# Kernel optimization log

Measured on AMD Instinct MI355X. Metric: run time of the kernel, lower is better.

## Reference

```python
import jax, jax.numpy as jnp
import numpy as np

B, S, E, H = 1, 2048, 512, 8
D = E // H
N = B * S
WIN_HALF = 32  # attention_window 64 -> +/-32
ALPHA = 0.1
LN_EPS = 1e-12
NEG_INF = -1e9


def _build_window_edges():
    # windowed graph: dst i attends to src j with |i-j| <= WIN_HALF, within each batch block
    i = np.arange(S)
    offs = np.arange(-WIN_HALF, WIN_HALF + 1)
    src = i[:, None] + offs[None, :]
    dst = np.broadcast_to(i[:, None], src.shape)
    valid = (src >= 0) & (src < S)
    src, dst = src[valid], dst[valid]
    srcs, dsts = [], []
    for b in range(B):
        srcs.append(src + b * S)
        dsts.append(dst + b * S)
    return (np.concatenate(srcs).astype(np.int32),
            np.concatenate(dsts).astype(np.int32))


def setup_inputs() -> dict:
    key = jax.random.key(0)
    ks = jax.random.split(key, 12)
    sc = 1.0 / np.sqrt(E)
    src_np, dst_np = _build_window_edges()
    return {
        "hidden_states": jax.random.normal(ks[0], (B, S, E), dtype=jnp.float32),
        "attention_mask": jnp.zeros((B, S), dtype=jnp.float32),
        "edge_src": jnp.asarray(src_np),
        "edge_dst": jnp.asarray(dst_np),
        "Wq": jax.random.normal(ks[1], (E, E), dtype=jnp.float32) * sc,
        "bq": jnp.zeros((E,), dtype=jnp.float32),
        "Wk": jax.random.normal(ks[2], (E, E), dtype=jnp.float32) * sc,
        "bk": jnp.zeros((E,), dtype=jnp.float32),
        "Wv": jax.random.normal(ks[3], (E, E), dtype=jnp.float32) * sc,
        "bv": jnp.zeros((E,), dtype=jnp.float32),
        "Wo": jax.random.normal(ks[4], (E, E), dtype=jnp.float32) * sc,
        "bo": jnp.zeros((E,), dtype=jnp.float32),
        "ln_g": jnp.ones((E,), dtype=jnp.float32),
        "ln_b": jnp.zeros((E,), dtype=jnp.float32),
    }


def reference(hidden_states, attention_mask, edge_src, edge_dst,
              Wq, bq, Wk, bk, Wv, bv, Wo, bo, ln_g, ln_b):
    x = hidden_states  # (B,S,E); node ordering n = b*S + s (matches torch reshape)
    q = ((x @ Wq + bq) / jnp.sqrt(jnp.asarray(D, x.dtype))).reshape(N, H, D)
    k = (x @ Wk + bk).reshape(N, H, D)
    v = (x @ Wv + bv).reshape(N, H, D)

    mask = (attention_mask >= 0).reshape(N)  # bool per node

    # u_dot_v('k','q','score'): per-edge, per-head dot product
    score = jnp.einsum('ehd,ehd->eh', k[edge_src], q[edge_dst])  # (Eg,H)
    score = jnp.where(mask[edge_src][:, None], score, NEG_INF)

    # edge_softmax over incoming edges of each destination node
    smax = jax.ops.segment_max(score, edge_dst, num_segments=N)
    p = jnp.exp(score - smax[edge_dst])
    denom = jax.ops.segment_sum(p, edge_dst, num_segments=N)
    p = p / denom[edge_dst]  # (Eg,H)

    # 5 diffusion steps: h <- A h, blended with residual v (dropout off in eval)
    h = v
    for _ in range(5):
        m = h[edge_src] * p[:, :, None]                      # u_mul_e
        h = jax.ops.segment_sum(m, edge_dst, num_segments=N)  # sum('m','h')
        h = (1.0 - ALPHA) * h + ALPHA * v

    attn = h.reshape(B, S, E)

    # DiffuserSelfOutput: dense -> residual add -> LayerNorm
    y = attn @ Wo + bo + hidden_states
    mu = y.mean(-1, keepdims=True)
    var = ((y - mu) ** 2).mean(-1, keepdims=True)
    out = (y - mu) * jax.lax.rsqrt(var + LN_EPS) * ln_g + ln_b
    return out
```

## Files before the change

### kernel.cpp

```cpp
#include <hip/hip_runtime.h>
#include <math.h>

#define S_LEN 2048
#define E_DIM 512
#define NE (S_LEN * E_DIM)
#define H_NUM 8
#define WH 32
#define NOFF 65
#define PROW (H_NUM * NOFF)
#define PN (S_LEN * PROW)

typedef float f32x4 __attribute__((ext_vector_type(4)));
typedef short short8 __attribute__((ext_vector_type(8)));

__device__ __forceinline__ unsigned short f2bf(float f) {
    union { float f; unsigned u; } cv; cv.f = f;
    unsigned u = cv.u;
    u += 0x7fffu + ((u >> 16) & 1u);
    return (unsigned short)(u >> 16);
}
__device__ __forceinline__ unsigned pk2(float x, float y) {
    return (unsigned)f2bf(x) | ((unsigned)f2bf(y) << 16);
}

__device__ __forceinline__ void mfma_gemm_f32(
    const float* __restrict__ A, const float* __restrict__ W,
    const float* __restrict__ bias, float* __restrict__ C,
    float scale, int m0, int n0)
{
    __shared__ unsigned short As[64 * 40];
    __shared__ unsigned short Bs[64 * 40];
    const int tid = threadIdx.x;
    const int lane = tid & 63, wave = tid >> 6;
    const int quad = lane >> 4, l16 = lane & 15;
    const int wr = (wave >> 1) * 32, wc = (wave & 1) * 32;
    const int ar = tid >> 2, ac = (tid & 3) * 8;
    const int bn = tid & 63, bk0 = (tid >> 6) * 8;

    f32x4 acc00 = {0.f,0.f,0.f,0.f}, acc01 = acc00, acc10 = acc00, acc11 = acc00;

    for (int kk = 0; kk < E_DIM; kk += 32) {
        float4 a0 = *(const float4*)(A + (size_t)(m0 + ar) * E_DIM + kk + ac);
        float4 a1 = *(const float4*)(A + (size_t)(m0 + ar) * E_DIM + kk + ac + 4);
        float b[8];
#pragma unroll
        for (int j = 0; j < 8; ++j)
            b[j] = W[(size_t)(kk + bk0 + j) * E_DIM + n0 + bn];
        __syncthreads();
        uint4 ap; ap.x = pk2(a0.x, a0.y); ap.y = pk2(a0.z, a0.w);
        ap.z = pk2(a1.x, a1.y); ap.w = pk2(a1.z, a1.w);
        *(uint4*)(As + ar * 40 + ac) = ap;
        uint4 bp; bp.x = pk2(b[0], b[1]); bp.y = pk2(b[2], b[3]);
        bp.z = pk2(b[4], b[5]); bp.w = pk2(b[6], b[7]);
        *(uint4*)(Bs + bn * 40 + bk0) = bp;
        __syncthreads();
        short8 fa0 = *(const short8*)(As + (wr + l16) * 40 + quad * 8);
        short8 fa1 = *(const short8*)(As + (wr + 16 + l16) * 40 + quad * 8);
        short8 fb0 = *(const short8*)(Bs + (wc + l16) * 40 + quad * 8);
        short8 fb1 = *(const short8*)(Bs + (wc + 16 + l16) * 40 + quad * 8);
        acc00 = __builtin_amdgcn_mfma_f32_16x16x32_bf16(fa0, fb0, acc00, 0, 0, 0);
        acc01 = __builtin_amdgcn_mfma_f32_16x16x32_bf16(fa0, fb1, acc01, 0, 0, 0);
        acc10 = __builtin_amdgcn_mfma_f32_16x16x32_bf16(fa1, fb0, acc10, 0, 0, 0);
        acc11 = __builtin_amdgcn_mfma_f32_16x16x32_bf16(fa1, fb1, acc11, 0, 0, 0);
    }

#pragma unroll
    for (int mi = 0; mi < 2; ++mi) {
#pragma unroll
        for (int ni = 0; ni < 2; ++ni) {
            f32x4 a = (mi == 0) ? ((ni == 0) ? acc00 : acc01)
                                : ((ni == 0) ? acc10 : acc11);
            int n = n0 + wc + ni * 16 + l16;
            float bval = bias[n];
#pragma unroll
            for (int r = 0; r < 4; ++r) {
                int m = m0 + wr + mi * 16 + quad * 4 + r;
                C[(size_t)m * E_DIM + n] = (a[r] + bval) * scale;
            }
        }
    }
}

__global__ __launch_bounds__(256)
void qkv_gemm(const float* __restrict__ x,
              const float* __restrict__ Wq, const float* __restrict__ bq,
              const float* __restrict__ Wk, const float* __restrict__ bk,
              const float* __restrict__ Wv, const float* __restrict__ bv,
              float* __restrict__ q, float* __restrict__ k, float* __restrict__ v)
{
    const float* W; const float* b; float* o; float sc;
    if (blockIdx.z == 0)      { W = Wq; b = bq; o = q; sc = 0.125f; }
    else if (blockIdx.z == 1) { W = Wk; b = bk; o = k; sc = 1.0f; }
    else                      { W = Wv; b = bv; o = v; sc = 1.0f; }
    mfma_gemm_f32(x, W, b, o, sc, blockIdx.y * 64, blockIdx.x * 64);
}

#define SDN 32
__global__ __launch_bounds__(256)
void scores_d1(const float* __restrict__ q, const float* __restrict__ k,
               const float* __restrict__ v, const float* __restrict__ amask,
               float* __restrict__ P, float* __restrict__ hA)
{
    const int i0 = blockIdx.x * SDN;
    const int h  = blockIdx.y;
    const int tid = threadIdx.x;
    __shared__ float ks[96 * 68];
    __shared__ float am[96];
    __shared__ float sc[SDN * 66];
    __shared__ float smx[SDN], sidn[SDN];
    __shared__ float ps[SDN * NOFF];

    for (int e = tid; e < 96 * 16; e += 256) {
        int lr = e >> 4, c4 = e & 15;
        int j = i0 - WH + lr;
        int jc = min(max(j, 0), S_LEN - 1);
        *(float4*)(ks + lr * 68 + c4 * 4) =
            *(const float4*)(k + (size_t)jc * E_DIM + h * 64 + c4 * 4);
    }
    if (tid < 96) {
        int j = i0 - WH + tid;
        am[tid] = (j >= 0 && j < S_LEN) ? amask[j] : -1.0f;
    }

    const int dst = tid >> 3;
    const int og  = tid & 7;
    float4 qreg[16];
    {
        const float4* qrow = (const float4*)(q + (size_t)(i0 + dst) * E_DIM + h * 64);
#pragma unroll
        for (int t = 0; t < 16; ++t) qreg[t] = qrow[t];
    }
    __syncthreads();

    for (int off = og; off < NOFF; off += 8) {
        int j = i0 + dst + off - WH;
        float s;
        if (j < 0 || j >= S_LEN) {
            s = -INFINITY;
        } else {
            int lr = dst + off;
            const float4* kr = (const float4*)(ks + lr * 68);
            float acc = 0.f;
#pragma unroll
            for (int t = 0; t < 16; ++t) {
                float4 a = qreg[t], bb = kr[t];
                acc += a.x * bb.x + a.y * bb.y + a.z * bb.z + a.w * bb.w;
            }
            s = (am[lr] >= 0.f) ? acc : -1e9f;
        }
        sc[dst * 66 + off] = s;
    }
    __syncthreads();

    for (int e = tid; e < 96 * 16; e += 256) {
        int lr = e >> 4, c4 = e & 15;
        int j = i0 - WH + lr;
        int jc = min(max(j, 0), S_LEN - 1);
        *(float4*)(ks + lr * 68 + c4 * 4) =
            *(const float4*)(v + (size_t)jc * E_DIM + h * 64 + c4 * 4);
    }
    if (tid < SDN) {
        float mx = -INFINITY;
        for (int o = 0; o < NOFF; ++o) mx = fmaxf(mx, sc[tid * 66 + o]);
        float dn = 0.f;
        for (int o = 0; o < NOFF; ++o) dn += expf(sc[tid * 66 + o] - mx);
        smx[tid] = mx; sidn[tid] = 1.f / dn;
    }
    __syncthreads();

    for (int e = tid; e < SDN * NOFF; e += 256) {
        int d = e / NOFF, off = e - d * NOFF;
        float pv = expf(sc[d * 66 + off] - smx[d]) * sidn[d];
        P[(size_t)(i0 + d) * PROW + h * NOFF + off] = pv;
        ps[e] = pv;
    }
    __syncthreads();

    {
        const int ci = tid & 15;
        const int ob = (tid >> 4) * 2;
        float4 a0 = {0,0,0,0}, a1 = a0;
        for (int lr = ob; lr < ob + 66; ++lr) {
            float4 hval = *(const float4*)(ks + lr * 68 + ci * 4);
            int o0 = lr - ob;
            if (o0 <= 64) {
                float p = ps[ob * NOFF + o0];
                a0.x += p * hval.x; a0.y += p * hval.y; a0.z += p * hval.z; a0.w += p * hval.w;
            }
            int o1 = o0 - 1;
            if ((unsigned)o1 <= 64u) {
                float p = ps[(ob + 1) * NOFF + o1];
                a1.x += p * hval.x; a1.y += p * hval.y; a1.z += p * hval.z; a1.w += p * hval.w;
            }
        }
#pragma unroll
        for (int r = 0; r < 2; ++r) {
            float4 a = r ? a1 : a0;
            float4 vv = *(const float4*)(ks + (WH + ob + r) * 68 + ci * 4);
            float4 o;
            o.x = 0.9f * a.x + 0.1f * vv.x;
            o.y = 0.9f * a.y + 0.1f * vv.y;
            o.z = 0.9f * a.z + 0.1f * vv.z;
            o.w = 0.9f * a.w + 0.1f * vv.w;
            *(float4*)(hA + (size_t)(i0 + ob + r) * E_DIM + h * 64 + ci * 4) = o;
        }
    }
}

__global__ __launch_bounds__(512)
void diffuse3m(const float* __restrict__ hin, const float* __restrict__ v,
               const float* __restrict__ P, float* __restrict__ hout)
{
    __shared__ unsigned short inT[64 * 264];
    __shared__ unsigned short m1T[64 * 200];
    __shared__ unsigned short ps[192 * 66];
    unsigned short* m2T = inT;
    const int i0 = blockIdx.x * 64;
    const int h  = blockIdx.y;
    const int c0 = h * 64;
    const int tid  = threadIdx.x;
    const int lane = tid & 63, wave = tid >> 6;
    const int quad = lane >> 4, l16 = lane & 15;

    for (int e = tid; e < 128 * 16; e += 512) {
        int rp = (e >> 4) * 2, c4 = (e & 15) * 4;
        int ja = min(max(i0 - 96 + rp,     0), S_LEN - 1);
        int jb = min(max(i0 - 96 + rp + 1, 0), S_LEN - 1);
        float4 ha = *(const float4*)(hin + (size_t)ja * E_DIM + c0 + c4);
        float4 hb = *(const float4*)(hin + (size_t)jb * E_DIM + c0 + c4);
        *(unsigned*)(inT + (c4 + 0) * 264 + rp) = pk2(ha.x, hb.x);
        *(unsigned*)(inT + (c4 + 1) * 264 + rp) = pk2(ha.y, hb.y);
        *(unsigned*)(inT + (c4 + 2) * 264 + rp) = pk2(ha.z, hb.z);
        *(unsigned*)(inT + (c4 + 3) * 264 + rp) = pk2(ha.w, hb.w);
    }
    for (int e = tid; e < 192 * 33; e += 512) {
        int mr = e / 33, t = e - mr * 33;
        int jc = min(max(i0 - 64 + mr, 0), S_LEN - 1);
        const float* pr = P + (size_t)jc * PROW + h * NOFF;
        if (t < 32)
            *(unsigned*)(ps + mr * 66 + t * 2) = pk2(pr[t * 2], pr[t * 2 + 1]);
        else
            ps[mr * 66 + 64] = f2bf(pr[64]);
    }
    __syncthreads();

#pragma unroll
    for (int uu = 0; uu < 3; ++uu) {
        int u = wave + uu * 8;
        int mtb = (u >> 1) * 16;
        int ntb = (u & 1) * 32;
        f32x4 a0 = {0.f,0.f,0.f,0.f}, a1 = a0;
        int ks0 = mtb >> 5;
        const int m = mtb + l16;
#pragma unroll
        for (int t = 0; t < 3; ++t) {
            int k0q = (ks0 + t) * 32 + quad * 8;
            short8 fa;
#pragma unroll
            for (int j = 0; j < 8; ++j) {
                int idx = k0q + j - m;
                int idc = min(max(idx, 0), 64);
                unsigned short pv = ps[m * 66 + idc];
                fa[j] = ((unsigned)idx <= 64u) ? (short)pv : (short)0;
            }
            short8 fb0 = *(const short8*)(inT + (ntb + l16) * 264 + k0q);
            short8 fb1 = *(const short8*)(inT + (ntb + 16 + l16) * 264 + k0q);
            a0 = __builtin_amdgcn_mfma_f32_16x16x32_bf16(fa, fb0, a0, 0, 0, 0);
            a1 = __builtin_amdgcn_mfma_f32_16x16x32_bf16(fa, fb1, a1, 0, 0, 0);
        }
#pragma unroll
        for (int nt = 0; nt < 2; ++nt) {
            f32x4 a = nt ? a1 : a0;
            int n = ntb + nt * 16 + l16;
            float o[4];
#pragma unroll
            for (int r = 0; r < 4; ++r) {
                int gm = min(max(i0 - 64 + mtb + quad * 4 + r, 0), S_LEN - 1);
                o[r] = 0.9f * a[r] + 0.1f * v[(size_t)gm * E_DIM + c0 + n];
            }
            *(unsigned*)(m1T + n * 200 + mtb + quad * 4)     = pk2(o[0], o[1]);
            *(unsigned*)(m1T + n * 200 + mtb + quad * 4 + 2) = pk2(o[2], o[3]);
        }
    }
    __syncthreads();

#pragma unroll
    for (int uu = 0; uu < 2; ++uu) {
        int u = wave + uu * 8;
        int mtb = (u >> 1) * 16;
        int ntb = (u & 1) * 32;
        f32x4 a0 = {0.f,0.f,0.f,0.f}, a1 = a0;
        int ks0 = mtb >> 5;
        const int m = mtb + l16;
#pragma unroll
        for (int t = 0; t < 3; ++t) {
            int k0q = (ks0 + t) * 32 + quad * 8;
            short8 fa;
#pragma unroll
            for (int j = 0; j < 8; ++j) {
                int idx = k0q + j - m;
                int idc = min(max(idx, 0), 64);
                unsigned short pv = ps[(m + 32) * 66 + idc];
                fa[j] = ((unsigned)idx <= 64u) ? (short)pv : (short)0;
            }
            short8 fb0 = *(const short8*)(m1T + (ntb + l16) * 200 + k0q);
            short8 fb1 = *(const short8*)(m1T + (ntb + 16 + l16) * 200 + k0q);
            a0 = __builtin_amdgcn_mfma_f32_16x16x32_bf16(fa, fb0, a0, 0, 0, 0);
            a1 = __builtin_amdgcn_mfma_f32_16x16x32_bf16(fa, fb1, a1, 0, 0, 0);
        }
        __syncthreads();
#pragma unroll
        for (int nt = 0; nt < 2; ++nt) {
            f32x4 a = nt ? a1 : a0;
            int n = ntb + nt * 16 + l16;
            float o[4];
#pragma unroll
            for (int r = 0; r < 4; ++r) {
                int gm = min(max(i0 - 32 + mtb + quad * 4 + r, 0), S_LEN - 1);
                o[r] = 0.9f * a[r] + 0.1f * v[(size_t)gm * E_DIM + c0 + n];
            }
            *(unsigned*)(m2T + n * 136 + mtb + quad * 4)     = pk2(o[0], o[1]);
            *(unsigned*)(m2T + n * 136 + mtb + quad * 4 + 2) = pk2(o[2], o[3]);
        }
    }
    __syncthreads();

    {
        int u = wave;
        int mtb = (u >> 1) * 16;
        int ntb = (u & 1) * 32;
        f32x4 a0 = {0.f,0.f,0.f,0.f}, a1 = a0;
        int ks0 = mtb >> 5;
        const int m = mtb + l16;
#pragma unroll
        for (int t = 0; t < 3; ++t) {
            int k0q = (ks0 + t) * 32 + quad * 8;
            short8 fa;
#pragma unroll
            for (int j = 0; j < 8; ++j) {
                int idx = k0q + j - m;
                int idc = min(max(idx, 0), 64);
                unsigned short pv = ps[(m + 64) * 66 + idc];
                fa[j] = ((unsigned)idx <= 64u) ? (short)pv : (short)0;
            }
            short8 fb0 = *(const short8*)(m2T + (ntb + l16) * 136 + k0q);
            short8 fb1 = *(const short8*)(m2T + (ntb + 16 + l16) * 136 + k0q);
            a0 = __builtin_amdgcn_mfma_f32_16x16x32_bf16(fa, fb0, a0, 0, 0, 0);
            a1 = __builtin_amdgcn_mfma_f32_16x16x32_bf16(fa, fb1, a1, 0, 0, 0);
        }
#pragma unroll
        for (int nt = 0; nt < 2; ++nt) {
            f32x4 a = nt ? a1 : a0;
            int n = ntb + nt * 16 + l16;
#pragma unroll
            for (int r = 0; r < 4; ++r) {
                int gm = i0 + mtb + quad * 4 + r;
                size_t base = (size_t)gm * E_DIM + c0 + n;
                hout[base] = 0.9f * a[r] + 0.1f * v[base];
            }
        }
    }
}

__global__ __launch_bounds__(512)
void oln4(const float* __restrict__ h4, const float* __restrict__ v,
          const float* __restrict__ P, const float* __restrict__ Wo,
          const float* __restrict__ bo, const float* __restrict__ x,
          const float* __restrict__ g, const float* __restrict__ lb,
          float* __restrict__ out)
{
    __shared__ unsigned short As16[16 * 520];
    __shared__ unsigned short Bs2[2][512 * 40];
    __shared__ float rsum[8][16], rsq[8][16];
    unsigned short* h4T  = &Bs2[0][0];
    unsigned short* ps16 = &Bs2[0][0] + 26624;

    const int tid = threadIdx.x;
    const int lane = tid & 63, wave = tid >> 6;
    const int quad = lane >> 4, l16 = lane & 15;
    const int m0 = blockIdx.x * 16;
    const int n = tid;

    for (int e = tid; e < 16 * 260; e += 512) {
        int mr = e / 260, t = e - mr * 260;
        const float* pr = P + (size_t)(m0 + mr) * PROW;
        *(unsigned*)(ps16 + mr * 528 + t * 2) = pk2(pr[t * 2], pr[t * 2 + 1]);
    }

    for (int hc = 0; hc < 2; ++hc) {
        for (int e = tid; e < 64 * 64; e += 512) {
            int r = e & 63, c4 = (e >> 6) * 4;
            int row = min(max(m0 - 32 + r, 0), S_LEN - 1);
            float4 hv = *(const float4*)(h4 + (size_t)row * E_DIM + hc * 256 + c4);
            h4T[(c4 + 0) * 104 + r] = f2bf(hv.x);
            h4T[(c4 + 1) * 104 + r] = f2bf(hv.y);
            h4T[(c4 + 2) * 104 + r] = f2bf(hv.z);
            h4T[(c4 + 3) * 104 + r] = f2bf(hv.w);
        }
        for (int e = tid; e < 32 * 64; e += 512) {
            int r = 64 + (e & 31), c4 = (e >> 5) * 4;
            int row = min(max(m0 - 32 + r, 0), S_LEN - 1);
            float4 hv = *(const float4*)(h4 + (size_t)row * E_DIM + hc * 256 + c4);
            h4T[(c4 + 0) * 104 + r] = f2bf(hv.x);
            h4T[(c4 + 1) * 104 + r] = f2bf(hv.y);
            h4T[(c4 + 2) * 104 + r] = f2bf(hv.z);
            h4T[(c4 + 3) * 104 + r] = f2bf(hv.w);
        }
        __syncthreads();

        {
            const int hd = hc * 4 + (wave >> 1);
            short8 fa[3];
#pragma unroll
            for (int t = 0; t < 3; ++t) {
                int k0q = t * 32 + quad * 8;
#pragma unroll
                for (int j = 0; j < 8; ++j) {
                    int idx = k0q + j - l16;
                    int idc = min(max(idx, 0), 64);
                    unsigned short pv = ps16[l16 * 528 + hd * NOFF + idc];
                    fa[t][j] = ((unsigned)idx <= 64u) ? (short)pv : (short)0;
                }
            }
#pragma unroll
            for (int nt = 0; nt < 2; ++nt) {
                int lc = wave * 32 + nt * 16;
                f32x4 ba = {0.f, 0.f, 0.f, 0.f};
#pragma unroll
                for (int t = 0; t < 3; ++t) {
                    short8 fb = *(const short8*)(h4T + (lc + l16) * 104 + t * 32 + quad * 8);
                    ba = __builtin_amdgcn_mfma_f32_16x16x32_bf16(fa[t], fb, ba, 0, 0, 0);
                }
                int gcol = hc * 256 + lc + l16;
#pragma unroll
                for (int r = 0; r < 4; ++r) {
                    int m = quad * 4 + r;
                    float vv = v[(size_t)(m0 + m) * E_DIM + gcol];
                    As16[m * 520 + gcol] = f2bf(0.9f * ba[r] + 0.1f * vv);
                }
            }
        }
        __syncthreads();
    }

    {
        float w0[32];
#pragma unroll
        for (int j = 0; j < 32; ++j)
            w0[j] = Wo[(size_t)j * E_DIM + n];
#pragma unroll
        for (int t = 0; t < 4; ++t) {
            uint4 bp;
            bp.x = pk2(w0[t*8+0], w0[t*8+1]); bp.y = pk2(w0[t*8+2], w0[t*8+3]);
            bp.z = pk2(w0[t*8+4], w0[t*8+5]); bp.w = pk2(w0[t*8+6], w0[t*8+7]);
            *(uint4*)(&Bs2[0][0] + n * 40 + t * 8) = bp;
        }
    }

    f32x4 acc[4];
#pragma unroll
    for (int t = 0; t < 4; ++t) acc[t] = (f32x4){0.f,0.f,0.f,0.f};

#pragma unroll 2
    for (int it = 0; it < 16; ++it) {
        float wn[32];
        if (it < 15) {
#pragma unroll
            for (int j = 0; j < 32; ++j)
                wn[j] = Wo[(size_t)((it + 1) * 32 + j) * E_DIM + n];
        }
        __syncthreads();

        short8 fa = *(const short8*)(As16 + l16 * 520 + it * 32 + quad * 8);
#pragma unroll
        for (int nt = 0; nt < 4; ++nt) {
            short8 fb = *(const short8*)(&Bs2[it & 1][0] +
                                         (wave * 64 + nt * 16 + l16) * 40 + quad * 8);
            acc[nt] = __builtin_amdgcn_mfma_f32_16x16x32_bf16(fa, fb, acc[nt], 0, 0, 0);
        }

        if (it < 15) {
#pragma unroll
            for (int t = 0; t < 4; ++t) {
                uint4 bp;
                bp.x = pk2(wn[t*8+0], wn[t*8+1]); bp.y = pk2(wn[t*8+2], wn[t*8+3]);
                bp.z = pk2(wn[t*8+4], wn[t*8+5]); bp.w = pk2(wn[t*8+6], wn[t*8+7]);
                *(uint4*)(&Bs2[(it + 1) & 1][0] + n * 40 + t * 8) = bp;
            }
        }
    }

    float s[4] = {0.f,0.f,0.f,0.f}, s2[4] = {0.f,0.f,0.f,0.f};
#pragma unroll
    for (int nt = 0; nt < 4; ++nt) {
        int nc = wave * 64 + nt * 16 + l16;
        float bv = bo[nc];
#pragma unroll
        for (int r = 0; r < 4; ++r) {
            int m = m0 + quad * 4 + r;
            float vl = acc[nt][r] + bv + x[(size_t)m * E_DIM + nc];
            acc[nt][r] = vl;
            s[r] += vl; s2[r] += vl * vl;
        }
    }
#pragma unroll
    for (int o = 1; o < 16; o <<= 1) {
#pragma unroll
        for (int r = 0; r < 4; ++r) {
            s[r]  += __shfl_xor(s[r], o, 64);
            s2[r] += __shfl_xor(s2[r], o, 64);
        }
    }
    if (l16 == 0) {
#pragma unroll
        for (int r = 0; r < 4; ++r) {
            rsum[wave][quad * 4 + r] = s[r];
            rsq[wave][quad * 4 + r]  = s2[r];
        }
    }
    __syncthreads();
    float mu[4], rs[4];
#pragma unroll
    for (int r = 0; r < 4; ++r) {
        int rl = quad * 4 + r;
        float tot = 0.f, tot2 = 0.f;
#pragma unroll
        for (int w = 0; w < 8; ++w) { tot += rsum[w][rl]; tot2 += rsq[w][rl]; }
        float m_ = tot * (1.f / 512.f);
        float var = tot2 * (1.f / 512.f) - m_ * m_;
        mu[r] = m_; rs[r] = rsqrtf(var + 1e-12f);
    }
#pragma unroll
    for (int nt = 0; nt < 4; ++nt) {
        int nc = wave * 64 + nt * 16 + l16;
        float gv = g[nc], bbv = lb[nc];
#pragma unroll
        for (int r = 0; r < 4; ++r) {
            int m = m0 + quad * 4 + r;
            out[(size_t)m * E_DIM + nc] = (acc[nt][r] - mu[r]) * rs[r] * gv + bbv;
        }
    }
}

extern "C" void kernel_launch(void* const* d_in, const int* in_sizes, int n_in,
                              void* d_out, int out_size, void* d_ws, size_t ws_size,
                              hipStream_t stream)
{
    const float* x     = (const float*)d_in[0];
    const float* amask = (const float*)d_in[1];
    const float* Wq = (const float*)d_in[4];
    const float* bq = (const float*)d_in[5];
    const float* Wk = (const float*)d_in[6];
    const float* bk = (const float*)d_in[7];
    const float* Wv = (const float*)d_in[8];
    const float* bv = (const float*)d_in[9];
    const float* Wo = (const float*)d_in[10];
    const float* bo = (const float*)d_in[11];
    const float* lng = (const float*)d_in[12];
    const float* lnb = (const float*)d_in[13];
    float* out = (float*)d_out;

    float* ws = (float*)d_ws;
    float* q  = ws;
    float* k  = ws + (size_t)NE;
    float* v  = ws + (size_t)2 * NE;
    float* P  = ws + (size_t)3 * NE;
    float* hA = ws + (size_t)3 * NE + PN;
    float* hB = hA + (size_t)NE;

    qkv_gemm<<<dim3(8, 32, 3), 256, 0, stream>>>(x, Wq, bq, Wk, bk, Wv, bv, q, k, v);

    scores_d1<<<dim3(64, 8), 256, 0, stream>>>(q, k, v, amask, P, hA);

    diffuse3m<<<dim3(32, 8), 512, 0, stream>>>(hA, v, P, hB);

    oln4<<<128, 512, 0, stream>>>(hB, v, P, Wo, bo, x, lng, lnb, out);
}
```

Measured before the change: 170.7 us.

## Double-buffer QKV GEMM tiles, register-resident softmax, LDS-only barriers in output GEMM

The QKV projection GEMM now double-buffers its shared-memory tiles and prefetches global loads two iterations ahead, so each step needs one barrier that waits only on LDS operations. The scores kernel keeps scores in registers and computes the softmax max and sum with warp shuffles across the 8 lanes per destination, removing the shared score buffer, one barrier and the serial per-row loop. The output GEMM drops the barrier at the top of each iteration in favour of an LGKM-only barrier after the LDS writes, and fully unrolls the loop. The costs are higher register pressure from the prefetch buffers and unrolling, and the risk of ordering hazards if the custom barrier does not cover every outstanding memory operation.

```diff
diff --git a/kernel.cpp b/kernel.cpp
--- a/kernel.cpp
+++ b/kernel.cpp
@@ -23,13 +23,20 @@
     return (unsigned)f2bf(x) | ((unsigned)f2bf(y) << 16);
 }
 
+#define LGKM_BARRIER() do {                                   \
+    __builtin_amdgcn_sched_barrier(0);                        \
+    asm volatile("s_waitcnt lgkmcnt(0)" ::: "memory");        \
+    __builtin_amdgcn_s_barrier();                             \
+    __builtin_amdgcn_sched_barrier(0);                        \
+} while (0)
+
 __device__ __forceinline__ void mfma_gemm_f32(
     const float* __restrict__ A, const float* __restrict__ W,
     const float* __restrict__ bias, float* __restrict__ C,
     float scale, int m0, int n0)
 {
-    __shared__ unsigned short As[64 * 40];
-    __shared__ unsigned short Bs[64 * 40];
+    __shared__ unsigned short As[2][64 * 40];
+    __shared__ unsigned short Bs[2][64 * 40];
     const int tid = threadIdx.x;
     const int lane = tid & 63, wave = tid >> 6;
     const int quad = lane >> 4, l16 = lane & 15;
@@ -39,30 +46,58 @@
 
     f32x4 acc00 = {0.f,0.f,0.f,0.f}, acc01 = acc00, acc10 = acc00, acc11 = acc00;
 
-    for (int kk = 0; kk < E_DIM; kk += 32) {
-        float4 a0 = *(const float4*)(A + (size_t)(m0 + ar) * E_DIM + kk + ac);
-        float4 a1 = *(const float4*)(A + (size_t)(m0 + ar) * E_DIM + kk + ac + 4);
-        float b[8];
-#pragma unroll
-        for (int j = 0; j < 8; ++j)
-            b[j] = W[(size_t)(kk + bk0 + j) * E_DIM + n0 + bn];
-        __syncthreads();
-        uint4 ap; ap.x = pk2(a0.x, a0.y); ap.y = pk2(a0.z, a0.w);
-        ap.z = pk2(a1.x, a1.y); ap.w = pk2(a1.z, a1.w);
-        *(uint4*)(As + ar * 40 + ac) = ap;
-        uint4 bp; bp.x = pk2(b[0], b[1]); bp.y = pk2(b[2], b[3]);
-        bp.z = pk2(b[4], b[5]); bp.w = pk2(b[6], b[7]);
-        *(uint4*)(Bs + bn * 40 + bk0) = bp;
-        __syncthreads();
-        short8 fa0 = *(const short8*)(As + (wr + l16) * 40 + quad * 8);
-        short8 fa1 = *(const short8*)(As + (wr + 16 + l16) * 40 + quad * 8);
-        short8 fb0 = *(const short8*)(Bs + (wc + l16) * 40 + quad * 8);
-        short8 fb1 = *(const short8*)(Bs + (wc + 16 + l16) * 40 + quad * 8);
+    const float* Arow = A + (size_t)(m0 + ar) * E_DIM;
+
+    float4 a0r[2], a1r[2];
+    float  br[2][8];
+
+#define QLOAD(s_, i_) do {                                                    \
+        int kk_ = (i_) * 32;                                                  \
+        a0r[s_] = *(const float4*)(Arow + kk_ + ac);                          \
+        a1r[s_] = *(const float4*)(Arow + kk_ + ac + 4);                      \
+        _Pragma("unroll")                                                     \
+        for (int j_ = 0; j_ < 8; ++j_)                                        \
+            br[s_][j_] = W[(size_t)(kk_ + bk0 + j_) * E_DIM + n0 + bn];       \
+    } while (0)
+
+#define QPACK(s_, b_) do {                                                    \
+        uint4 ap_;                                                            \
+        ap_.x = pk2(a0r[s_].x, a0r[s_].y); ap_.y = pk2(a0r[s_].z, a0r[s_].w); \
+        ap_.z = pk2(a1r[s_].x, a1r[s_].y); ap_.w = pk2(a1r[s_].z, a1r[s_].w); \
+        *(uint4*)(&As[b_][0] + ar * 40 + ac) = ap_;                           \
+        uint4 bp_;                                                            \
+        bp_.x = pk2(br[s_][0], br[s_][1]); bp_.y = pk2(br[s_][2], br[s_][3]); \
+        bp_.z = pk2(br[s_][4], br[s_][5]); bp_.w = pk2(br[s_][6], br[s_][7]); \
+        *(uint4*)(&Bs[b_][0] + bn * 40 + bk0) = bp_;                          \
+    } while (0)
+
+    QLOAD(0, 0);
+    QPACK(0, 0);
+    QLOAD(1, 1);
+    LGKM_BARRIER();
+
+#pragma unroll
+    for (int it = 0; it < 16; ++it) {
+        if (it < 14) QLOAD(it & 1, it + 2);
+
+        const unsigned short* Ab = &As[it & 1][0];
+        const unsigned short* Bb = &Bs[it & 1][0];
+        short8 fa0 = *(const short8*)(Ab + (wr + l16) * 40 + quad * 8);
+        short8 fa1 = *(const short8*)(Ab + (wr + 16 + l16) * 40 + quad * 8);
+        short8 fb0 = *(const short8*)(Bb + (wc + l16) * 40 + quad * 8);
+        short8 fb1 = *(const short8*)(Bb + (wc + 16 + l16) * 40 + quad * 8);
         acc00 = __builtin_amdgcn_mfma_f32_16x16x32_bf16(fa0, fb0, acc00, 0, 0, 0);
         acc01 = __builtin_amdgcn_mfma_f32_16x16x32_bf16(fa0, fb1, acc01, 0, 0, 0);
         acc10 = __builtin_amdgcn_mfma_f32_16x16x32_bf16(fa1, fb0, acc10, 0, 0, 0);
         acc11 = __builtin_amdgcn_mfma_f32_16x16x32_bf16(fa1, fb1, acc11, 0, 0, 0);
-    }
+
+        if (it < 15) {
+            QPACK((it + 1) & 1, (it + 1) & 1);
+            LGKM_BARRIER();
+        }
+    }
+#undef QLOAD
+#undef QPACK
 
 #pragma unroll
     for (int mi = 0; mi < 2; ++mi) {
@@ -106,8 +141,6 @@
     const int tid = threadIdx.x;
     __shared__ float ks[96 * 68];
     __shared__ float am[96];
-    __shared__ float sc[SDN * 66];
-    __shared__ float smx[SDN], sidn[SDN];
     __shared__ float ps[SDN * NOFF];
 
     for (int e = tid; e < 96 * 16; e += 256) {
@@ -132,23 +165,25 @@
     }
     __syncthreads();
 
-    for (int off = og; off < NOFF; off += 8) {
+    float sreg[9];
+#pragma unroll
+    for (int t = 0; t < 9; ++t) sreg[t] = -INFINITY;
+#pragma unroll
+    for (int t = 0; t < 9; ++t) {
+        int off = og + 8 * t;
+        if (off > 64) break;
         int j = i0 + dst + off - WH;
-        float s;
-        if (j < 0 || j >= S_LEN) {
-            s = -INFINITY;
-        } else {
+        if (j >= 0 && j < S_LEN) {
             int lr = dst + off;
             const float4* kr = (const float4*)(ks + lr * 68);
             float acc = 0.f;
 #pragma unroll
-            for (int t = 0; t < 16; ++t) {
-                float4 a = qreg[t], bb = kr[t];
+            for (int u = 0; u < 16; ++u) {
+                float4 a = qreg[u], bb = kr[u];
                 acc += a.x * bb.x + a.y * bb.y + a.z * bb.z + a.w * bb.w;
             }
-            s = (am[lr] >= 0.f) ? acc : -1e9f;
-        }
-        sc[dst * 66 + off] = s;
+            sreg[t] = (am[lr] >= 0.f) ? acc : -1e9f;
+        }
     }
     __syncthreads();
 
@@ -159,20 +194,28 @@
         *(float4*)(ks + lr * 68 + c4 * 4) =
             *(const float4*)(v + (size_t)jc * E_DIM + h * 64 + c4 * 4);
     }
-    if (tid < SDN) {
-        float mx = -INFINITY;
-        for (int o = 0; o < NOFF; ++o) mx = fmaxf(mx, sc[tid * 66 + o]);
-        float dn = 0.f;
-        for (int o = 0; o < NOFF; ++o) dn += expf(sc[tid * 66 + o] - mx);
-        smx[tid] = mx; sidn[tid] = 1.f / dn;
-    }
-    __syncthreads();
-
-    for (int e = tid; e < SDN * NOFF; e += 256) {
-        int d = e / NOFF, off = e - d * NOFF;
-        float pv = expf(sc[d * 66 + off] - smx[d]) * sidn[d];
-        P[(size_t)(i0 + d) * PROW + h * NOFF + off] = pv;
-        ps[e] = pv;
+
+    float mx = sreg[0];
+#pragma unroll
+    for (int t = 1; t < 9; ++t) mx = fmaxf(mx, sreg[t]);
+#pragma unroll
+    for (int o = 1; o < 8; o <<= 1) mx = fmaxf(mx, __shfl_xor(mx, o, 64));
+    float dn = 0.f;
+#pragma unroll
+    for (int t = 0; t < 9; ++t) {
+        sreg[t] = expf(sreg[t] - mx);
+        dn += sreg[t];
+    }
+#pragma unroll
+    for (int o = 1; o < 8; o <<= 1) dn += __shfl_xor(dn, o, 64);
+    float rinv = 1.f / dn;
+#pragma unroll
+    for (int t = 0; t < 9; ++t) {
+        int off = og + 8 * t;
+        if (off > 64) break;
+        float pv = sreg[t] * rinv;
+        P[(size_t)(i0 + dst) * PROW + h * NOFF + off] = pv;
+        ps[dst * NOFF + off] = pv;
     }
     __syncthreads();
 
@@ -456,12 +499,13 @@
             *(uint4*)(&Bs2[0][0] + n * 40 + t * 8) = bp;
         }
     }
+    LGKM_BARRIER();
 
     f32x4 acc[4];
 #pragma unroll
     for (int t = 0; t < 4; ++t) acc[t] = (f32x4){0.f,0.f,0.f,0.f};
 
-#pragma unroll 2
+#pragma unroll
     for (int it = 0; it < 16; ++it) {
         float wn[32];
         if (it < 15) {
@@ -469,7 +513,6 @@
             for (int j = 0; j < 32; ++j)
                 wn[j] = Wo[(size_t)((it + 1) * 32 + j) * E_DIM + n];
         }
-        __syncthreads();
 
         short8 fa = *(const short8*)(As16 + l16 * 520 + it * 32 + quad * 8);
 #pragma unroll
@@ -487,6 +530,7 @@
                 bp.z = pk2(wn[t*8+4], wn[t*8+5]); bp.w = pk2(wn[t*8+6], wn[t*8+7]);
                 *(uint4*)(&Bs2[(it + 1) & 1][0] + n * 40 + t * 8) = bp;
             }
+            LGKM_BARRIER();
         }
     }
 
```

Result: faster. 165.3 us (-3.2%).
